# Optimization experiments

Measured on AMD Instinct MI355X. Metric: run time of the kernel, lower is better.

The kernel has to match this reference:

```python
import jax, jax.numpy as jnp
import numpy as np

N, E, F_NODE, F_EDGE, D, OUT, G = 32768, 98304, 32, 16, 64, 16, 64
EPS = 1e-5


def setup_inputs() -> dict:
    key = jax.random.key(0)
    ks = jax.random.split(key, 26)
    s = 0.05
    rn = lambda k, shp: jax.random.normal(k, shp, dtype=jnp.float32) * s
    return {
        "x": jax.random.normal(ks[0], (N, F_NODE), dtype=jnp.float32),
        "edge_attr": jax.random.normal(ks[1], (E, F_EDGE), dtype=jnp.float32),
        "edge_index": jax.random.randint(ks[2], (2, E), 0, N, dtype=jnp.int32),
        "batch": jnp.sort(jax.random.randint(ks[3], (N,), 0, G, dtype=jnp.int32)),
        # fc1
        "fc1_w": rn(ks[4], (F_NODE, D)), "fc1_b": jnp.zeros((D,), jnp.float32),
        # edge MLP 1 + NNConv1 root/bias
        "efc1_w1": rn(ks[5], (F_EDGE, D)), "efc1_b1": jnp.zeros((D,), jnp.float32),
        "efc1_w2": rn(ks[6], (D, D * D)), "efc1_b2": jnp.zeros((D * D,), jnp.float32),
        "root1": rn(ks[7], (D, D)), "bias1": jnp.zeros((D,), jnp.float32),
        "gn1_w": jnp.ones((D,), jnp.float32), "gn1_b": jnp.zeros((D,), jnp.float32),
        # edge MLP 2 + NNConv2 root/bias
        "efc2_w1": rn(ks[8], (F_EDGE, D)), "efc2_b1": jnp.zeros((D,), jnp.float32),
        "efc2_w2": rn(ks[9], (D, D * D)), "efc2_b2": jnp.zeros((D * D,), jnp.float32),
        "root2": rn(ks[10], (D, D)), "bias2": jnp.zeros((D,), jnp.float32),
        "gn2_w": jnp.ones((D,), jnp.float32), "gn2_b": jnp.zeros((D,), jnp.float32),
        # fc2
        "fc2_w": rn(ks[11], (D, OUT)), "fc2_b": jnp.zeros((OUT,), jnp.float32),
    }


def _nnconv(x, edge_index, edge_attr, w1, b1, w2, b2, root, bias):
    # edge MLP -> per-edge [D, D] weight
    h = jax.nn.relu(edge_attr @ w1 + b1)
    we = (h @ w2 + b2).reshape(-1, D, D)          # [E, D, D]
    src, dst = edge_index[0], edge_index[1]
    msg = jnp.einsum('ei,eio->eo', x[src], we)    # per-edge 1xD @ DxD
    agg = jax.ops.segment_sum(msg, dst, num_segments=x.shape[0])  # aggr='add'
    return agg + x @ root + bias


def _graph_layernorm(x, w, b):
    # PyG LayerNorm(mode='graph') with batch=None: global mean/std over all elems
    xc = x - x.mean()
    return xc / (jnp.std(xc) + EPS) * w + b


def _global_mean_pool(h, batch, n_graphs):
    sums = jax.ops.segment_sum(h, batch, num_segments=n_graphs)
    cnt = jax.ops.segment_sum(jnp.ones((h.shape[0],), h.dtype), batch, num_segments=n_graphs)
    return sums / jnp.clip(cnt, 1.0)[:, None]


def reference(x, edge_attr, edge_index, batch,
              fc1_w, fc1_b,
              efc1_w1, efc1_b1, efc1_w2, efc1_b2, root1, bias1, gn1_w, gn1_b,
              efc2_w1, efc2_b1, efc2_w2, efc2_b2, root2, bias2, gn2_w, gn2_b,
              fc2_w, fc2_b):
    hx = x @ fc1_w + fc1_b
    h = jax.nn.relu(_graph_layernorm(
        _nnconv(hx, edge_index, edge_attr, efc1_w1, efc1_b1, efc1_w2, efc1_b2, root1, bias1),
        gn1_w, gn1_b))
    h = jax.nn.relu(_graph_layernorm(
        _nnconv(h, edge_index, edge_attr, efc2_w1, efc2_b1, efc2_w2, efc2_b2, root2, bias2),
        gn2_w, gn2_b))
    pooled = _global_mean_pool(h, batch, G)       # [G, D]
    return pooled @ fc2_w + fc2_b                 # [G, OUT]
```

## Files before the change

kernel.cpp:

```cpp
#include <hip/hip_runtime.h>
#include <hip/hip_bf16.h>

#define NN    32768
#define EE    98304
#define FN    32
#define FEDGE 16
#define DD    64
#define OUTD  16
#define GG    64
#define EPSL  1e-5f

typedef __attribute__((ext_vector_type(8))) short bf16x8;
typedef __attribute__((ext_vector_type(4))) float f32x4;

__device__ __forceinline__ void gload_lds16(const void* g, void* l) {
    __builtin_amdgcn_global_load_lds(
        (const __attribute__((address_space(1))) void*)g,
        (__attribute__((address_space(3))) void*)l, 16, 0, 0);
}

__device__ __forceinline__ ushort f2bf(float f) {
    __hip_bfloat16 b = __float2bfloat16(f);
    return *(ushort*)&b;
}

__global__ __launch_bounds__(256) void k_fc1(const float* __restrict__ x,
                                             const float* __restrict__ w,
                                             const float* __restrict__ b,
                                             float* __restrict__ hx) {
    int t = threadIdx.x;
    int d = t & 63;
    int n = blockIdx.x * 4 + (t >> 6);
    const float* xr = x + n * FN;
    float acc = b[d];
    #pragma unroll
    for (int i = 0; i < FN; ++i) acc += xr[i] * w[i * DD + d];
    hx[n * DD + d] = acc;
}

__global__ __launch_bounds__(256) void k_mlp(const float* __restrict__ ea,
                                             const float* __restrict__ w1,
                                             const float* __restrict__ b1,
                                             __hip_bfloat16* __restrict__ het) {
    __shared__ float eas[256][17];
    int t = threadIdx.x;
    int e0 = blockIdx.x * 256;
    const float4* src = (const float4*)(ea + e0 * FEDGE);
    #pragma unroll
    for (int j = 0; j < 4; ++j) {
        float4 v = src[t + 256 * j];
        int f = (t + 256 * j) * 4;
        int e = f >> 4, i = f & 15;
        eas[e][i] = v.x; eas[e][i + 1] = v.y; eas[e][i + 2] = v.z; eas[e][i + 3] = v.w;
    }
    __syncthreads();
    int e = e0 + t;
    float a[FEDGE];
    #pragma unroll
    for (int i = 0; i < FEDGE; ++i) a[i] = eas[t][i];
    for (int k = 0; k < DD; ++k) {
        float acc = b1[k];
        #pragma unroll
        for (int i = 0; i < FEDGE; ++i) acc += a[i] * w1[i * DD + k];
        acc = fmaxf(acc, 0.0f);
        het[k * EE + e] = __float2bfloat16(acc);
    }
    het[DD * EE + e] = __float2bfloat16(1.0f);
}

__global__ __launch_bounds__(256) void k_prep(const float* __restrict__ w2,
                                              const float* __restrict__ b2,
                                              ushort* __restrict__ w2t) {
    int s = blockIdx.x;
    const float* src = (s < 64) ? (w2 + s * 4096) : b2;
    int t = threadIdx.x;
    int o = t >> 2;
    #pragma unroll
    for (int j = 0; j < 16; ++j) {
        int i = (t & 3) * 16 + j;
        w2t[s * 4096 + o * 64 + (i ^ ((o & 7) << 3))] = f2bf(src[i * 64 + o]);
    }
}

__global__ __launch_bounds__(256) void k_agginit(const float* __restrict__ xin,
                                                 const float* __restrict__ root,
                                                 const float* __restrict__ bias,
                                                 float* __restrict__ agg) {
    int t = threadIdx.x;
    int o = t & 63;
    int n = blockIdx.x * 4 + (t >> 6);
    const float* xr = xin + n * DD;
    float acc = bias[o];
    #pragma unroll
    for (int i = 0; i < DD; ++i) acc += xr[i] * root[i * DD + o];
    agg[n * DD + o] = acc;
}

__global__ __launch_bounds__(256) void k_conv(const float* __restrict__ xs,
                                              const __hip_bfloat16* __restrict__ het,
                                              const ushort* __restrict__ w2t,
                                              const int* __restrict__ ei,
                                              float* __restrict__ agg) {
    __shared__ __align__(16) ushort hs[65 * 128];
    __shared__ __align__(16) ushort w2s[2 * 4096];

    const int t   = threadIdx.x;
    const int l   = t & 63;
    const int w   = t >> 6;
    const int q   = l >> 4;
    const int r16 = l & 15;
    const int q8  = q * 8;
    const int e0  = blockIdx.x * 128;

    float xsr[2][16];
    #pragma unroll
    for (int sm = 0; sm < 2; ++sm) {
        int em = e0 + w * 32 + sm * 16 + r16;
        int sn = ei[em];
        const float4* xr = (const float4*)(xs + sn * DD);
        float4 a0 = xr[q * 2], a1 = xr[q * 2 + 1];
        float4 b0 = xr[8 + q * 2], b1 = xr[8 + q * 2 + 1];
        xsr[sm][0] = a0.x;  xsr[sm][1] = a0.y;  xsr[sm][2]  = a0.z;  xsr[sm][3]  = a0.w;
        xsr[sm][4] = a1.x;  xsr[sm][5] = a1.y;  xsr[sm][6]  = a1.z;  xsr[sm][7]  = a1.w;
        xsr[sm][8] = b0.x;  xsr[sm][9] = b0.y;  xsr[sm][10] = b0.z;  xsr[sm][11] = b0.w;
        xsr[sm][12] = b1.x; xsr[sm][13] = b1.y; xsr[sm][14] = b1.z;  xsr[sm][15] = b1.w;
    }

    uint* hsu = (uint*)hs;
    for (int j = t; j < 65 * 64; j += 256) {
        int k = j >> 6, eu = j & 63;
        hsu[j] = ((const uint*)(het + k * EE + e0))[eu];
    }

    asm volatile("s_waitcnt vmcnt(0) lgkmcnt(0)" ::: "memory");

    uint boff[2][4];
    #pragma unroll
    for (int nt = 0; nt < 4; ++nt) {
        int o = nt * 16 + r16;
        int x = (o & 7) << 3;
        #pragma unroll
        for (int p = 0; p < 2; ++p)
            boff[p][nt] = (uint)(o * 64 + ((p * 32 + q8) ^ x));
    }

    f32x4 acc[2][4];
    #pragma unroll
    for (int sm = 0; sm < 2; ++sm)
        #pragma unroll
        for (int nt = 0; nt < 4; ++nt)
            acc[sm][nt] = (f32x4){0.f, 0.f, 0.f, 0.f};

    auto stage = [&](int s) {
        #pragma unroll
        for (int c = 0; c < 2; ++c)
            gload_lds16(w2t + s * 4096 + w * 1024 + c * 512 + l * 8,
                        &w2s[(s & 1) * 4096 + w * 1024 + c * 512]);
    };

    stage(0);
    for (int s = 0; s < 65; ++s) {
        if (s < 64) {
            stage(s + 1);
            asm volatile("s_waitcnt vmcnt(2)" ::: "memory");
        } else {
            asm volatile("s_waitcnt vmcnt(0)" ::: "memory");
        }
        __builtin_amdgcn_s_barrier();
        __builtin_amdgcn_sched_barrier(0);

        const ushort* bp = &w2s[(s & 1) * 4096];

        float hv[2];
        #pragma unroll
        for (int sm = 0; sm < 2; ++sm) {
            ushort hu = hs[s * 128 + w * 32 + sm * 16 + r16];
            union { uint u; float f; } cv; cv.u = ((uint)hu) << 16;
            hv[sm] = cv.f;
        }

        #pragma unroll
        for (int p = 0; p < 2; ++p) {
            bf16x8 bfr[4];
            #pragma unroll
            for (int nt = 0; nt < 4; ++nt)
                bfr[nt] = *(const bf16x8*)(bp + boff[p][nt]);
            #pragma unroll
            for (int sm = 0; sm < 2; ++sm) {
                union { bf16x8 v; ushort u[8]; } af;
                #pragma unroll
                for (int j = 0; j < 8; ++j)
                    af.u[j] = f2bf(hv[sm] * xsr[sm][p * 8 + j]);
                #pragma unroll
                for (int nt = 0; nt < 4; ++nt)
                    acc[sm][nt] = __builtin_amdgcn_mfma_f32_16x16x32_bf16(
                        af.v, bfr[nt], acc[sm][nt], 0, 0, 0);
            }
        }
        asm volatile("s_waitcnt lgkmcnt(0)" ::: "memory");
        __builtin_amdgcn_s_barrier();
    }

    #pragma unroll
    for (int sm = 0; sm < 2; ++sm) {
        #pragma unroll
        for (int rr = 0; rr < 4; ++rr) {
            int em = e0 + w * 32 + sm * 16 + q * 4 + rr;
            int dn = ei[EE + em];
            float* ar = agg + dn * DD + r16;
            #pragma unroll
            for (int nt = 0; nt < 4; ++nt)
                atomicAdd(ar + nt * 16, acc[sm][nt][rr]);
        }
    }
}

__global__ __launch_bounds__(256) void k_lnred(const float* __restrict__ v,
                                               float* __restrict__ stats) {
    int t = threadIdx.x;
    int base = blockIdx.x * 4096 + t;
    float s = 0.0f, s2 = 0.0f;
    #pragma unroll
    for (int j = 0; j < 16; ++j) {
        float x = v[base + j * 256];
        s += x; s2 += x * x;
    }
    #pragma unroll
    for (int off = 32; off > 0; off >>= 1) {
        s  += __shfl_down(s, off, 64);
        s2 += __shfl_down(s2, off, 64);
    }
    __shared__ float ps[8];
    int w = t >> 6;
    if ((t & 63) == 0) { ps[w] = s; ps[4 + w] = s2; }
    __syncthreads();
    if (t == 0) {
        atomicAdd(&stats[0], ps[0] + ps[1] + ps[2] + ps[3]);
        atomicAdd(&stats[1], ps[4] + ps[5] + ps[6] + ps[7]);
    }
}

__global__ __launch_bounds__(256) void k_lnapply(float* __restrict__ v,
                                                 const float* __restrict__ stats,
                                                 const float* __restrict__ gw,
                                                 const float* __restrict__ gb) {
    const float M = (float)(NN * DD);
    float mean = stats[0] / M;
    float var  = stats[1] / M - mean * mean;
    float rden = 1.0f / (sqrtf(fmaxf(var, 0.0f)) + EPSL);
    int t = threadIdx.x;
    int base = blockIdx.x * 1024 + t;
    #pragma unroll
    for (int j = 0; j < 4; ++j) {
        int idx = base + j * 256;
        int d = idx & 63;
        float x = v[idx];
        v[idx] = fmaxf((x - mean) * rden * gw[d] + gb[d], 0.0f);
    }
}

__global__ __launch_bounds__(256) void k_pool(const float* __restrict__ h,
                                              const int* __restrict__ batch,
                                              float* __restrict__ pool,
                                              float* __restrict__ cnt) {
    int t = threadIdx.x;
    int d = t & 63;
    int ln = t >> 6;
    int n0 = blockIdx.x * 256;
    float s = 0.0f, sc = 0.0f;
    int cur = batch[n0 + ln];
    for (int j = 0; j < 64; ++j) {
        int n = n0 + ln + j * 4;
        int b = batch[n];
        if (b != cur) {
            atomicAdd(&pool[cur * DD + d], s);
            if (d == 0) atomicAdd(&cnt[cur], sc);
            s = 0.0f; sc = 0.0f; cur = b;
        }
        s  += h[n * DD + d];
        sc += 1.0f;
    }
    atomicAdd(&pool[cur * DD + d], s);
    if (d == 0) atomicAdd(&cnt[cur], sc);
}

__global__ __launch_bounds__(256) void k_fc2(const float* __restrict__ pool,
                                             const float* __restrict__ cnt,
                                             const float* __restrict__ w,
                                             const float* __restrict__ b,
                                             float* __restrict__ out) {
    int t = threadIdx.x;
    int o = t & 15;
    int g0 = t >> 4;
    #pragma unroll
    for (int gg = 0; gg < 4; ++gg) {
        int g = g0 + gg * 16;
        float inv = 1.0f / fmaxf(cnt[g], 1.0f);
        float acc = b[o];
        for (int d = 0; d < DD; ++d)
            acc += pool[g * DD + d] * inv * w[d * OUTD + o];
        out[g * OUTD + o] = acc;
    }
}

extern "C" void kernel_launch(void* const* d_in, const int* in_sizes, int n_in,
                              void* d_out, int out_size, void* d_ws, size_t ws_size,
                              hipStream_t stream) {
    const float* x       = (const float*)d_in[0];
    const float* ea      = (const float*)d_in[1];
    const int*   ei      = (const int*)d_in[2];
    const int*   batch   = (const int*)d_in[3];
    const float* fc1_w   = (const float*)d_in[4];
    const float* fc1_b   = (const float*)d_in[5];
    const float* e1w1    = (const float*)d_in[6];
    const float* e1b1    = (const float*)d_in[7];
    const float* e1w2    = (const float*)d_in[8];
    const float* e1b2    = (const float*)d_in[9];
    const float* root1   = (const float*)d_in[10];
    const float* bias1   = (const float*)d_in[11];
    const float* gn1w    = (const float*)d_in[12];
    const float* gn1b    = (const float*)d_in[13];
    const float* e2w1    = (const float*)d_in[14];
    const float* e2b1    = (const float*)d_in[15];
    const float* e2w2    = (const float*)d_in[16];
    const float* e2b2    = (const float*)d_in[17];
    const float* root2   = (const float*)d_in[18];
    const float* bias2   = (const float*)d_in[19];
    const float* gn2w    = (const float*)d_in[20];
    const float* gn2b    = (const float*)d_in[21];
    const float* fc2_w   = (const float*)d_in[22];
    const float* fc2_b   = (const float*)d_in[23];
    float* out = (float*)d_out;

    char* ws = (char*)d_ws;
    float*          hx    = (float*)(ws);
    float*          agg1  = (float*)(ws + 8388608);
    __hip_bfloat16* het   = (__hip_bfloat16*)(ws + 16777216);
    ushort*         w2t   = (ushort*)(ws + 29556736);
    float*          pool  = (float*)(ws + 30089216);
    float*          cnt   = (float*)(ws + 30105600);
    float*          stats = (float*)(ws + 30105856);
    float*          agg2  = hx;

    hipMemsetAsync(ws + 30089216, 0, 16384 + 256 + 16, stream);

    k_fc1<<<NN / 4, 256, 0, stream>>>(x, fc1_w, fc1_b, hx);
    k_mlp<<<EE / 256, 256, 0, stream>>>(ea, e1w1, e1b1, het);
    k_prep<<<65, 256, 0, stream>>>(e1w2, e1b2, w2t);
    k_agginit<<<NN / 4, 256, 0, stream>>>(hx, root1, bias1, agg1);
    k_conv<<<EE / 128, 256, 0, stream>>>(hx, het, w2t, ei, agg1);
    k_lnred<<<(NN * DD) / 4096, 256, 0, stream>>>(agg1, stats);
    k_lnapply<<<(NN * DD) / 1024, 256, 0, stream>>>(agg1, stats, gn1w, gn1b);

    k_mlp<<<EE / 256, 256, 0, stream>>>(ea, e2w1, e2b1, het);
    k_prep<<<65, 256, 0, stream>>>(e2w2, e2b2, w2t);
    k_agginit<<<NN / 4, 256, 0, stream>>>(agg1, root2, bias2, agg2);
    k_conv<<<EE / 128, 256, 0, stream>>>(agg1, het, w2t, ei, agg2);
    k_lnred<<<(NN * DD) / 4096, 256, 0, stream>>>(agg2, stats + 2);
    k_lnapply<<<(NN * DD) / 1024, 256, 0, stream>>>(agg2, stats + 2, gn2w, gn2b);

    k_pool<<<NN / 256, 256, 0, stream>>>(agg2, batch, pool, cnt);
    k_fc2<<<1, 256, 0, stream>>>(pool, cnt, fc2_w, fc2_b, out);
}
```

Before: 444.1 us.

## Fuse root matmul into neighbours, switch conv to fp16 with 384-edge tiles

Fuses the root-weight node transform into the fc1 and layernorm-apply kernels, and fuses the final layernorm-apply into the pooling kernel, which removes several full passes over node features. The edge conv now uses fp16 MFMA with packed half2 multiplies, where it used bf16 with scalar conversions. Each block now covers 384 edges instead of 128, so every staged weight slice is reused across more edges. The larger register footprint (launch_bounds 256,1) lowers occupancy and gives fewer blocks (256 on 256 CUs), and fp16 carries a different range and precision risk.

```diff
diff --git a/kernel.cpp b/kernel.cpp
--- a/kernel.cpp
+++ b/kernel.cpp
@@ -1,5 +1,6 @@
 #include <hip/hip_runtime.h>
 #include <hip/hip_bf16.h>
+#include <hip/hip_fp16.h>
 
 #define NN    32768
 #define EE    98304
@@ -9,8 +10,9 @@
 #define OUTD  16
 #define GG    64
 #define EPSL  1e-5f
-
-typedef __attribute__((ext_vector_type(8))) short bf16x8;
+#define EB    384
+
+typedef __attribute__((ext_vector_type(8))) _Float16 f16x8;
 typedef __attribute__((ext_vector_type(4))) float f32x4;
 
 __device__ __forceinline__ void gload_lds16(const void* g, void* l) {
@@ -19,29 +21,38 @@
         (__attribute__((address_space(3))) void*)l, 16, 0, 0);
 }
 
-__device__ __forceinline__ ushort f2bf(float f) {
-    __hip_bfloat16 b = __float2bfloat16(f);
-    return *(ushort*)&b;
-}
-
-__global__ __launch_bounds__(256) void k_fc1(const float* __restrict__ x,
-                                             const float* __restrict__ w,
-                                             const float* __restrict__ b,
-                                             float* __restrict__ hx) {
-    int t = threadIdx.x;
-    int d = t & 63;
-    int n = blockIdx.x * 4 + (t >> 6);
+__global__ __launch_bounds__(256) void k_fc1agg(const float* __restrict__ x,
+                                                const float* __restrict__ w1,
+                                                const float* __restrict__ b1,
+                                                const float* __restrict__ root,
+                                                const float* __restrict__ rbias,
+                                                float* __restrict__ hx,
+                                                float* __restrict__ agg) {
+    __shared__ float rowbuf[4][64];
+    int t = threadIdx.x, d = t & 63, wv = t >> 6;
+    int n = blockIdx.x * 4 + wv;
     const float* xr = x + n * FN;
-    float acc = b[d];
-    #pragma unroll
-    for (int i = 0; i < FN; ++i) acc += xr[i] * w[i * DD + d];
+    float acc = b1[d];
+    #pragma unroll
+    for (int i = 0; i < FN; ++i) acc += xr[i] * w1[i * DD + d];
     hx[n * DD + d] = acc;
+    rowbuf[wv][d] = acc;
+    __syncthreads();
+    float a0 = rbias[d], a1 = 0.f, a2 = 0.f, a3 = 0.f;
+    #pragma unroll
+    for (int i = 0; i < DD; i += 4) {
+        a0 += rowbuf[wv][i]     * root[i * DD + d];
+        a1 += rowbuf[wv][i + 1] * root[(i + 1) * DD + d];
+        a2 += rowbuf[wv][i + 2] * root[(i + 2) * DD + d];
+        a3 += rowbuf[wv][i + 3] * root[(i + 3) * DD + d];
+    }
+    agg[n * DD + d] = (a0 + a1) + (a2 + a3);
 }
 
 __global__ __launch_bounds__(256) void k_mlp(const float* __restrict__ ea,
                                              const float* __restrict__ w1,
                                              const float* __restrict__ b1,
-                                             __hip_bfloat16* __restrict__ het) {
+                                             __half* __restrict__ het) {
     __shared__ float eas[256][17];
     int t = threadIdx.x;
     int e0 = blockIdx.x * 256;
@@ -63,14 +74,14 @@
         #pragma unroll
         for (int i = 0; i < FEDGE; ++i) acc += a[i] * w1[i * DD + k];
         acc = fmaxf(acc, 0.0f);
-        het[k * EE + e] = __float2bfloat16(acc);
-    }
-    het[DD * EE + e] = __float2bfloat16(1.0f);
+        het[k * EE + e] = __float2half_rn(acc);
+    }
+    het[DD * EE + e] = __float2half_rn(1.0f);
 }
 
 __global__ __launch_bounds__(256) void k_prep(const float* __restrict__ w2,
                                               const float* __restrict__ b2,
-                                              ushort* __restrict__ w2t) {
+                                              __half* __restrict__ w2t) {
     int s = blockIdx.x;
     const float* src = (s < 64) ? (w2 + s * 4096) : b2;
     int t = threadIdx.x;
@@ -78,31 +89,17 @@
     #pragma unroll
     for (int j = 0; j < 16; ++j) {
         int i = (t & 3) * 16 + j;
-        w2t[s * 4096 + o * 64 + (i ^ ((o & 7) << 3))] = f2bf(src[i * 64 + o]);
-    }
-}
-
-__global__ __launch_bounds__(256) void k_agginit(const float* __restrict__ xin,
-                                                 const float* __restrict__ root,
-                                                 const float* __restrict__ bias,
+        w2t[s * 4096 + o * 64 + (i ^ ((o & 7) << 3))] = __float2half_rn(src[i * 64 + o]);
+    }
+}
+
+__global__ __launch_bounds__(256, 1) void k_conv(const float* __restrict__ xs,
+                                                 const __half* __restrict__ het,
+                                                 const __half* __restrict__ w2t,
+                                                 const int* __restrict__ ei,
                                                  float* __restrict__ agg) {
-    int t = threadIdx.x;
-    int o = t & 63;
-    int n = blockIdx.x * 4 + (t >> 6);
-    const float* xr = xin + n * DD;
-    float acc = bias[o];
-    #pragma unroll
-    for (int i = 0; i < DD; ++i) acc += xr[i] * root[i * DD + o];
-    agg[n * DD + o] = acc;
-}
-
-__global__ __launch_bounds__(256) void k_conv(const float* __restrict__ xs,
-                                              const __hip_bfloat16* __restrict__ het,
-                                              const ushort* __restrict__ w2t,
-                                              const int* __restrict__ ei,
-                                              float* __restrict__ agg) {
-    __shared__ __align__(16) ushort hs[65 * 128];
-    __shared__ __align__(16) ushort w2s[2 * 4096];
+    __shared__ __align__(16) __half hs[65 * EB];
+    __shared__ __align__(16) __half w2s[2 * 4096];
 
     const int t   = threadIdx.x;
     const int l   = t & 63;
@@ -110,43 +107,44 @@
     const int q   = l >> 4;
     const int r16 = l & 15;
     const int q8  = q * 8;
-    const int e0  = blockIdx.x * 128;
-
-    float xsr[2][16];
-    #pragma unroll
-    for (int sm = 0; sm < 2; ++sm) {
-        int em = e0 + w * 32 + sm * 16 + r16;
+    const int e0  = blockIdx.x * EB;
+
+    __half2 xh[6][8];
+    #pragma unroll
+    for (int sm = 0; sm < 6; ++sm) {
+        int em = e0 + w * 96 + sm * 16 + r16;
         int sn = ei[em];
         const float4* xr = (const float4*)(xs + sn * DD);
         float4 a0 = xr[q * 2], a1 = xr[q * 2 + 1];
         float4 b0 = xr[8 + q * 2], b1 = xr[8 + q * 2 + 1];
-        xsr[sm][0] = a0.x;  xsr[sm][1] = a0.y;  xsr[sm][2]  = a0.z;  xsr[sm][3]  = a0.w;
-        xsr[sm][4] = a1.x;  xsr[sm][5] = a1.y;  xsr[sm][6]  = a1.z;  xsr[sm][7]  = a1.w;
-        xsr[sm][8] = b0.x;  xsr[sm][9] = b0.y;  xsr[sm][10] = b0.z;  xsr[sm][11] = b0.w;
-        xsr[sm][12] = b1.x; xsr[sm][13] = b1.y; xsr[sm][14] = b1.z;  xsr[sm][15] = b1.w;
-    }
-
-    uint* hsu = (uint*)hs;
-    for (int j = t; j < 65 * 64; j += 256) {
-        int k = j >> 6, eu = j & 63;
-        hsu[j] = ((const uint*)(het + k * EE + e0))[eu];
-    }
-
-    asm volatile("s_waitcnt vmcnt(0) lgkmcnt(0)" ::: "memory");
+        xh[sm][0] = __floats2half2_rn(a0.x, a0.y);
+        xh[sm][1] = __floats2half2_rn(a0.z, a0.w);
+        xh[sm][2] = __floats2half2_rn(a1.x, a1.y);
+        xh[sm][3] = __floats2half2_rn(a1.z, a1.w);
+        xh[sm][4] = __floats2half2_rn(b0.x, b0.y);
+        xh[sm][5] = __floats2half2_rn(b0.z, b0.w);
+        xh[sm][6] = __floats2half2_rn(b1.x, b1.y);
+        xh[sm][7] = __floats2half2_rn(b1.z, b1.w);
+    }
+
+    for (int j = t; j < 65 * 48; j += 256) {
+        int row = j / 48, col = j - row * 48;
+        ((uint4*)hs)[j] = ((const uint4*)(het + row * EE + e0))[col];
+    }
 
     uint boff[2][4];
     #pragma unroll
     for (int nt = 0; nt < 4; ++nt) {
         int o = nt * 16 + r16;
-        int x = (o & 7) << 3;
+        int xm = (o & 7) << 3;
         #pragma unroll
         for (int p = 0; p < 2; ++p)
-            boff[p][nt] = (uint)(o * 64 + ((p * 32 + q8) ^ x));
-    }
-
-    f32x4 acc[2][4];
-    #pragma unroll
-    for (int sm = 0; sm < 2; ++sm)
+            boff[p][nt] = (uint)(o * 64 + ((p * 32 + q8) ^ xm));
+    }
+
+    f32x4 acc[6][4];
+    #pragma unroll
+    for (int sm = 0; sm < 6; ++sm)
         #pragma unroll
         for (int nt = 0; nt < 4; ++nt)
             acc[sm][nt] = (f32x4){0.f, 0.f, 0.f, 0.f};
@@ -159,6 +157,8 @@
     };
 
     stage(0);
+    asm volatile("s_waitcnt vmcnt(0) lgkmcnt(0)" ::: "memory");
+
     for (int s = 0; s < 65; ++s) {
         if (s < 64) {
             stage(s + 1);
@@ -169,31 +169,28 @@
         __builtin_amdgcn_s_barrier();
         __builtin_amdgcn_sched_barrier(0);
 
-        const ushort* bp = &w2s[(s & 1) * 4096];
-
-        float hv[2];
-        #pragma unroll
-        for (int sm = 0; sm < 2; ++sm) {
-            ushort hu = hs[s * 128 + w * 32 + sm * 16 + r16];
-            union { uint u; float f; } cv; cv.u = ((uint)hu) << 16;
-            hv[sm] = cv.f;
-        }
+        const __half* bp = &w2s[(s & 1) * 4096];
+
+        __half2 hh[6];
+        #pragma unroll
+        for (int sm = 0; sm < 6; ++sm)
+            hh[sm] = __half2half2(hs[s * EB + w * 96 + sm * 16 + r16]);
 
         #pragma unroll
         for (int p = 0; p < 2; ++p) {
-            bf16x8 bfr[4];
+            f16x8 bfr[4];
             #pragma unroll
             for (int nt = 0; nt < 4; ++nt)
-                bfr[nt] = *(const bf16x8*)(bp + boff[p][nt]);
+                bfr[nt] = *(const f16x8*)(bp + boff[p][nt]);
             #pragma unroll
-            for (int sm = 0; sm < 2; ++sm) {
-                union { bf16x8 v; ushort u[8]; } af;
+            for (int sm = 0; sm < 6; ++sm) {
+                union { f16x8 v; __half2 h2[4]; } af;
                 #pragma unroll
-                for (int j = 0; j < 8; ++j)
-                    af.u[j] = f2bf(hv[sm] * xsr[sm][p * 8 + j]);
+                for (int jj = 0; jj < 4; ++jj)
+                    af.h2[jj] = __hmul2(hh[sm], xh[sm][p * 4 + jj]);
                 #pragma unroll
                 for (int nt = 0; nt < 4; ++nt)
-                    acc[sm][nt] = __builtin_amdgcn_mfma_f32_16x16x32_bf16(
+                    acc[sm][nt] = __builtin_amdgcn_mfma_f32_16x16x32_f16(
                         af.v, bfr[nt], acc[sm][nt], 0, 0, 0);
             }
         }
@@ -202,10 +199,10 @@
     }
 
     #pragma unroll
-    for (int sm = 0; sm < 2; ++sm) {
+    for (int sm = 0; sm < 6; ++sm) {
         #pragma unroll
         for (int rr = 0; rr < 4; ++rr) {
-            int em = e0 + w * 32 + sm * 16 + q * 4 + rr;
+            int em = e0 + w * 96 + sm * 16 + q * 4 + rr;
             int dn = ei[EE + em];
             float* ar = agg + dn * DD + r16;
             #pragma unroll
@@ -240,33 +237,52 @@
     }
 }
 
-__global__ __launch_bounds__(256) void k_lnapply(float* __restrict__ v,
-                                                 const float* __restrict__ stats,
-                                                 const float* __restrict__ gw,
-                                                 const float* __restrict__ gb) {
+__global__ __launch_bounds__(256) void k_lnagg(float* __restrict__ h1,
+                                               const float* __restrict__ stats,
+                                               const float* __restrict__ gw,
+                                               const float* __restrict__ gb,
+                                               const float* __restrict__ root,
+                                               const float* __restrict__ rbias,
+                                               float* __restrict__ agg2) {
     const float M = (float)(NN * DD);
     float mean = stats[0] / M;
     float var  = stats[1] / M - mean * mean;
     float rden = 1.0f / (sqrtf(fmaxf(var, 0.0f)) + EPSL);
-    int t = threadIdx.x;
-    int base = blockIdx.x * 1024 + t;
-    #pragma unroll
-    for (int j = 0; j < 4; ++j) {
-        int idx = base + j * 256;
-        int d = idx & 63;
-        float x = v[idx];
-        v[idx] = fmaxf((x - mean) * rden * gw[d] + gb[d], 0.0f);
-    }
-}
-
-__global__ __launch_bounds__(256) void k_pool(const float* __restrict__ h,
-                                              const int* __restrict__ batch,
-                                              float* __restrict__ pool,
-                                              float* __restrict__ cnt) {
+    __shared__ float rowbuf[4][64];
+    int t = threadIdx.x, d = t & 63, wv = t >> 6;
+    int n = blockIdx.x * 4 + wv;
+    float v = h1[n * DD + d];
+    float h = fmaxf((v - mean) * rden * gw[d] + gb[d], 0.0f);
+    h1[n * DD + d] = h;
+    rowbuf[wv][d] = h;
+    __syncthreads();
+    float a0 = rbias[d], a1 = 0.f, a2 = 0.f, a3 = 0.f;
+    #pragma unroll
+    for (int i = 0; i < DD; i += 4) {
+        a0 += rowbuf[wv][i]     * root[i * DD + d];
+        a1 += rowbuf[wv][i + 1] * root[(i + 1) * DD + d];
+        a2 += rowbuf[wv][i + 2] * root[(i + 2) * DD + d];
+        a3 += rowbuf[wv][i + 3] * root[(i + 3) * DD + d];
+    }
+    agg2[n * DD + d] = (a0 + a1) + (a2 + a3);
+}
+
+__global__ __launch_bounds__(256) void k_lnpool(const float* __restrict__ v,
+                                                const float* __restrict__ stats,
+                                                const float* __restrict__ gw,
+                                                const float* __restrict__ gb,
+                                                const int* __restrict__ batch,
+                                                float* __restrict__ pool,
+                                                float* __restrict__ cnt) {
+    const float M = (float)(NN * DD);
+    float mean = stats[0] / M;
+    float var  = stats[1] / M - mean * mean;
+    float rden = 1.0f / (sqrtf(fmaxf(var, 0.0f)) + EPSL);
     int t = threadIdx.x;
     int d = t & 63;
     int ln = t >> 6;
     int n0 = blockIdx.x * 256;
+    float gwd = gw[d] * rden, gbd = gb[d];
     float s = 0.0f, sc = 0.0f;
     int cur = batch[n0 + ln];
     for (int j = 0; j < 64; ++j) {
@@ -277,7 +293,7 @@
             if (d == 0) atomicAdd(&cnt[cur], sc);
             s = 0.0f; sc = 0.0f; cur = b;
         }
-        s  += h[n * DD + d];
+        s  += fmaxf((v[n * DD + d] - mean) * gwd + gbd, 0.0f);
         sc += 1.0f;
     }
     atomicAdd(&pool[cur * DD + d], s);
@@ -333,32 +349,29 @@
     float* out = (float*)d_out;
 
     char* ws = (char*)d_ws;
-    float*          hx    = (float*)(ws);
-    float*          agg1  = (float*)(ws + 8388608);
-    __hip_bfloat16* het   = (__hip_bfloat16*)(ws + 16777216);
-    ushort*         w2t   = (ushort*)(ws + 29556736);
-    float*          pool  = (float*)(ws + 30089216);
-    float*          cnt   = (float*)(ws + 30105600);
-    float*          stats = (float*)(ws + 30105856);
-    float*          agg2  = hx;
+    float*  hx    = (float*)(ws);
+    float*  agg1  = (float*)(ws + 8388608);
+    __half* het   = (__half*)(ws + 16777216);
+    __half* w2t   = (__half*)(ws + 29556736);
+    float*  pool  = (float*)(ws + 30089216);
+    float*  cnt   = (float*)(ws + 30105600);
+    float*  stats = (float*)(ws + 30105856);
+    float*  agg2  = hx;
 
     hipMemsetAsync(ws + 30089216, 0, 16384 + 256 + 16, stream);
 
-    k_fc1<<<NN / 4, 256, 0, stream>>>(x, fc1_w, fc1_b, hx);
+    k_fc1agg<<<NN / 4, 256, 0, stream>>>(x, fc1_w, fc1_b, root1, bias1, hx, agg1);
     k_mlp<<<EE / 256, 256, 0, stream>>>(ea, e1w1, e1b1, het);
     k_prep<<<65, 256, 0, stream>>>(e1w2, e1b2, w2t);
-    k_agginit<<<NN / 4, 256, 0, stream>>>(hx, root1, bias1, agg1);
-    k_conv<<<EE / 128, 256, 0, stream>>>(hx, het, w2t, ei, agg1);
+    k_conv<<<EE / EB, 256, 0, stream>>>(hx, het, w2t, ei, agg1);
     k_lnred<<<(NN * DD) / 4096, 256, 0, stream>>>(agg1, stats);
-    k_lnapply<<<(NN * DD) / 1024, 256, 0, stream>>>(agg1, stats, gn1w, gn1b);
+    k_lnagg<<<NN / 4, 256, 0, stream>>>(agg1, stats, gn1w, gn1b, root2, bias2, agg2);
 
     k_mlp<<<EE / 256, 256, 0, stream>>>(ea, e2w1, e2b1, het);
     k_prep<<<65, 256, 0, stream>>>(e2w2, e2b2, w2t);
-    k_agginit<<<NN / 4, 256, 0, stream>>>(agg1, root2, bias2, agg2);
-    k_conv<<<EE / 128, 256, 0, stream>>>(agg1, het, w2t, ei, agg2);
+    k_conv<<<EE / EB, 256, 0, stream>>>(agg1, het, w2t, ei, agg2);
     k_lnred<<<(NN * DD) / 4096, 256, 0, stream>>>(agg2, stats + 2);
-    k_lnapply<<<(NN * DD) / 1024, 256, 0, stream>>>(agg2, stats + 2, gn2w, gn2b);
-
-    k_pool<<<NN / 256, 256, 0, stream>>>(agg2, batch, pool, cnt);
+
+    k_lnpool<<<NN / 256, 256, 0, stream>>>(agg2, stats + 2, gn2w, gn2b, batch, pool, cnt);
     k_fc2<<<1, 256, 0, stream>>>(pool, cnt, fc2_w, fc2_b, out);
 }
```

After: 422.3 us. 1.05x faster.
